# Kernel tuning notes

Measured on AMD Instinct MI355X. Metric: run time of the kernel, lower is better.

The kernel has to match this reference:

```python
import jax, jax.numpy as jnp
import numpy as np

DIM = 768
NUM_EXPERTS = 1536
EXPERT_DIM = 64
NOISE_SCALE = 0.1
B, H, W = 1, 64, 64
N = B * H * W


def setup_inputs() -> dict:
    key = jax.random.key(0)
    ks = jax.random.split(key, 6)
    scaled = lambda k, shape, fan_in: (jax.random.normal(k, shape, jnp.float32) / np.sqrt(fan_in)).astype(jnp.float32)
    return {
        "x": jax.random.normal(ks[0], (B, H, W, DIM), jnp.float32),
        "noise": jax.random.normal(ks[1], (N, NUM_EXPERTS), jnp.float32),
        "gate_w": scaled(ks[2], (NUM_EXPERTS, DIM), DIM),
        "gate_b": jnp.zeros((NUM_EXPERTS,), jnp.float32),
        "expert_w": scaled(ks[3], (NUM_EXPERTS, EXPERT_DIM, DIM), DIM),  # torch Linear weight layout (out, in)
        "expert_b": jnp.zeros((NUM_EXPERTS, EXPERT_DIM), jnp.float32),
        "proj_w": scaled(ks[4], (DIM, EXPERT_DIM), EXPERT_DIM),
        "proj_b": jnp.zeros((DIM,), jnp.float32),
    }


def reference(x, noise, gate_w, gate_b, expert_w, expert_b, proj_w, proj_b):
    orig_shape = x.shape
    xf = x.reshape(-1, orig_shape[-1])  # (N, DIM)
    # Noisy gating
    scores = xf @ gate_w.T + gate_b + noise * NOISE_SCALE  # (N, E)
    gate_weights = jax.nn.softmax(scores, axis=-1)
    top_w, top_i = jax.lax.top_k(gate_weights, 1)  # (N, 1), (N, 1)
    idx = top_i[:, 0]  # (N,)
    # Gather only the selected expert per token (same math as the redundant
    # dense all-expert compute followed by a gather in the original).
    w_sel = expert_w[idx]  # (N, EXPERT_DIM, DIM)
    b_sel = expert_b[idx]  # (N, EXPERT_DIM)
    y = jnp.einsum('nd,nod->no', xf, w_sel) + b_sel  # (N, EXPERT_DIM)
    out_flat = (y @ proj_w.T + proj_b) * top_w  # (N, DIM); top_w broadcasts (N,1)
    return out_flat.reshape(orig_shape)
```

## Files before the change

kernel.cpp:

```cpp
#include <hip/hip_runtime.h>
#include <hip/hip_bf16.h>

#define NT 4096
#define DIM 768
#define NE 1536
#define ED 64
#define GAP_THR 8e-3f

typedef __attribute__((ext_vector_type(8))) short short8v;
typedef __attribute__((ext_vector_type(4))) float f32x4;

__device__ __forceinline__ unsigned short f2bf(float f) {
  unsigned int u = __float_as_uint(f);
  unsigned int r = (u + 0x7fffu + ((u >> 16) & 1u)) >> 16;
  return (unsigned short)r;
}
__device__ __forceinline__ float bf2f(unsigned short h) {
  return __uint_as_float(((unsigned int)h) << 16);
}

__device__ __forceinline__ void gload16(const void* g, void* l) {
  __builtin_amdgcn_global_load_lds((const __attribute__((address_space(1))) void*)g,
                                   (__attribute__((address_space(3))) void*)l, 16, 0, 0);
}

__device__ __forceinline__ void top2_merge(float& m1, int& i1, float& m2, int& i2,
                                           float om1, int oi1, float om2, int oi2) {
  if (om1 > m1 || (om1 == m1 && oi1 < i1)) {
    if (m1 > om2 || (m1 == om2 && i1 < oi2)) { m2 = m1; i2 = i1; }
    else { m2 = om2; i2 = oi2; }
    m1 = om1; i1 = oi1;
  } else {
    if (om1 > m2 || (om1 == m2 && oi1 < i2)) { m2 = om1; i2 = oi1; }
  }
}

__global__ __launch_bounds__(256) void split_all(
    const float* __restrict__ x, const float* __restrict__ gw,
    unsigned short* __restrict__ xhi, unsigned short* __restrict__ xlo,
    unsigned short* __restrict__ ghi, unsigned short* __restrict__ glo,
    int* __restrict__ rc_cnt) {
  if (blockIdx.x == 0 && threadIdx.x == 0) *rc_cnt = 0;
  const int nx4 = NT * DIM / 4;
  const int ng4 = NE * DIM / 4;
  int i = blockIdx.x * 256 + threadIdx.x;
  const float* src; unsigned short* hi; unsigned short* lo; int j;
  if (i < nx4) { src = x; hi = xhi; lo = xlo; j = i; }
  else { j = i - nx4; if (j >= ng4) return; src = gw; hi = ghi; lo = glo; }
  float4 v = ((const float4*)src)[j];
  unsigned short h0 = f2bf(v.x), h1 = f2bf(v.y), h2 = f2bf(v.z), h3 = f2bf(v.w);
  ((ushort4*)hi)[j] = make_ushort4(h0, h1, h2, h3);
  ((ushort4*)lo)[j] = make_ushort4(f2bf(v.x - bf2f(h0)), f2bf(v.y - bf2f(h1)),
                                   f2bf(v.z - bf2f(h2)), f2bf(v.w - bf2f(h3)));
}

__global__ __launch_bounds__(256) void gate_mfma(
    const unsigned short* __restrict__ xhi, const unsigned short* __restrict__ xlo,
    const unsigned short* __restrict__ ghi, const unsigned short* __restrict__ glo,
    const float* __restrict__ gb, const float* __restrict__ noise,
    float4* __restrict__ part_a, int* __restrict__ part_i2) {
  __shared__ __align__(16) unsigned short sA[2 * 128 * 32];
  __shared__ __align__(16) unsigned short sB[2 * 128 * 32];
  const int tid = threadIdx.x;
  const int w = tid >> 6, lane = tid & 63;
  const int wr = w >> 1, wc = w & 1;
  const int bm = blockIdx.x, bn = blockIdx.y;
  const int fr = lane & 15;
  const int fg = lane >> 4;
  const int gsw = fg ^ ((fr >> 1) & 3);

  f32x4 acc[4][4];
#pragma unroll
  for (int i = 0; i < 4; i++)
#pragma unroll
    for (int j = 0; j < 4; j++) acc[i][j] = (f32x4){0.f, 0.f, 0.f, 0.f};

  const size_t arow = (size_t)bm * 128 * DIM;
  const size_t brow = (size_t)bn * 128 * DIM;
  const int sr_lo = tid >> 2;
  const int sg = (tid & 3) ^ ((tid >> 3) & 3);

  for (int kt = 0; kt < DIM; kt += 32) {
    __syncthreads();
#pragma unroll
    for (int h = 0; h < 2; h++) {
      const int r = h * 64 + sr_lo;
      const size_t asrc = arow + (size_t)r * DIM + kt + sg * 8;
      const size_t bsrc = brow + (size_t)r * DIM + kt + sg * 8;
      const int dofs = h * 2048 + w * 512;
      gload16(xhi + asrc, &sA[dofs]);
      gload16(xlo + asrc, &sA[4096 + dofs]);
      gload16(ghi + bsrc, &sB[dofs]);
      gload16(glo + bsrc, &sB[4096 + dofs]);
    }
    __syncthreads();

    short8v ah[4], al[4], bh[4], bl[4];
#pragma unroll
    for (int mf = 0; mf < 4; mf++) {
      int ro = (wr * 64 + mf * 16 + fr) * 32 + gsw * 8;
      ah[mf] = *(const short8v*)&sA[ro];
      al[mf] = *(const short8v*)&sA[4096 + ro];
    }
#pragma unroll
    for (int nf = 0; nf < 4; nf++) {
      int ro = (wc * 64 + nf * 16 + fr) * 32 + gsw * 8;
      bh[nf] = *(const short8v*)&sB[ro];
      bl[nf] = *(const short8v*)&sB[4096 + ro];
    }
#pragma unroll
    for (int mf = 0; mf < 4; mf++)
#pragma unroll
      for (int nf = 0; nf < 4; nf++) {
        f32x4 c = acc[mf][nf];
        c = __builtin_amdgcn_mfma_f32_16x16x32_bf16(ah[mf], bh[nf], c, 0, 0, 0);
        c = __builtin_amdgcn_mfma_f32_16x16x32_bf16(ah[mf], bl[nf], c, 0, 0, 0);
        c = __builtin_amdgcn_mfma_f32_16x16x32_bf16(al[mf], bh[nf], c, 0, 0, 0);
        acc[mf][nf] = c;
      }
  }

  const int gm0 = bm * 128 + wr * 64;
  const int gn0 = bn * 128 + wc * 64;
  const int chunk = bn * 2 + wc;
  int gcol[4]; float gbv[4];
#pragma unroll
  for (int nf = 0; nf < 4; nf++) { gcol[nf] = gn0 + nf * 16 + fr; gbv[nf] = gb[gcol[nf]]; }
#pragma unroll
  for (int mf = 0; mf < 4; mf++) {
    float sv[4][4];
#pragma unroll
    for (int nf = 0; nf < 4; nf++)
#pragma unroll
      for (int reg = 0; reg < 4; reg++) {
        int gm = gm0 + mf * 16 + fg * 4 + reg;
        sv[nf][reg] = acc[mf][nf][reg] + gbv[nf] + 0.1f * noise[(size_t)gm * NE + gcol[nf]];
      }
#pragma unroll
    for (int reg = 0; reg < 4; reg++) {
      float m1 = sv[0][reg]; int i1 = gcol[0];
      float m2 = -3e38f; int i2 = 0x7fffffff;
#pragma unroll
      for (int nf = 1; nf < 4; nf++) {
        float v = sv[nf][reg]; int ii = gcol[nf];
        if (v > m1 || (v == m1 && ii < i1)) { m2 = m1; i2 = i1; m1 = v; i1 = ii; }
        else if (v > m2 || (v == m2 && ii < i2)) { m2 = v; i2 = ii; }
      }
#pragma unroll
      for (int off = 1; off <= 8; off <<= 1) {
        float om1 = __shfl_xor(m1, off, 64); int oi1 = __shfl_xor(i1, off, 64);
        float om2 = __shfl_xor(m2, off, 64); int oi2 = __shfl_xor(i2, off, 64);
        top2_merge(m1, i1, m2, i2, om1, oi1, om2, oi2);
      }
      float ssum = 0.f;
#pragma unroll
      for (int nf = 0; nf < 4; nf++) ssum += __expf(sv[nf][reg] - m1);
#pragma unroll
      for (int off = 1; off <= 8; off <<= 1) ssum += __shfl_xor(ssum, off, 64);
      if (fr == 0) {
        int gm = gm0 + mf * 16 + fg * 4 + reg;
        part_a[(size_t)gm * 24 + chunk] = make_float4(m1, m2, ssum, __int_as_float(i1));
        part_i2[(size_t)gm * 24 + chunk] = i2;
      }
    }
  }
}

__global__ __launch_bounds__(256) void finalize(
    const float4* __restrict__ part_a, const int* __restrict__ part_i2,
    float* __restrict__ topw, int* __restrict__ idx,
    int* __restrict__ rc_count, int* __restrict__ rc_n, int* __restrict__ rc_i2) {
  const int wv = threadIdx.x >> 6, lane = threadIdx.x & 63;
  const int n = blockIdx.x * 4 + wv;
  float m1 = -3e38f, m2 = -3e38f, lm1 = -3e38f, lsum = 0.f;
  int i1 = 0x7fffffff, i2 = 0x7fffffff;
  if (lane < 24) {
    float4 pa = part_a[(size_t)n * 24 + lane];
    m1 = pa.x; m2 = pa.y; lsum = pa.z; i1 = __float_as_int(pa.w);
    i2 = part_i2[(size_t)n * 24 + lane];
    lm1 = pa.x;
  }
#pragma unroll
  for (int off = 1; off <= 32; off <<= 1) {
    float om1 = __shfl_xor(m1, off, 64); int oi1 = __shfl_xor(i1, off, 64);
    float om2 = __shfl_xor(m2, off, 64); int oi2 = __shfl_xor(i2, off, 64);
    top2_merge(m1, i1, m2, i2, om1, oi1, om2, oi2);
  }
  float contrib = (lane < 24) ? __expf(lm1 - m1) * lsum : 0.f;
#pragma unroll
  for (int off = 1; off <= 32; off <<= 1) contrib += __shfl_xor(contrib, off, 64);
  if (lane == 0) {
    topw[n] = 1.0f / contrib;
    idx[n] = i1;
    if (m1 - m2 < GAP_THR) {
      int p = atomicAdd(rc_count, 1);
      rc_n[p] = n; rc_i2[p] = i2;
    }
  }
}

__global__ __launch_bounds__(256) void recheck(
    const float* __restrict__ x, const float* __restrict__ gw,
    const float* __restrict__ gb, const float* __restrict__ noise,
    const int* __restrict__ rc_n, const int* __restrict__ rc_i2,
    const int* __restrict__ rc_count, int* __restrict__ idx) {
  __shared__ float r1[4], r2[4];
  const int cnt = *rc_count;
  const int tid = threadIdx.x;
  const int w = tid >> 6, lane = tid & 63;
  for (int t = blockIdx.x; t < cnt; t += gridDim.x) {
    const int n = rc_n[t];
    const int e1 = idx[n], e2 = rc_i2[t];
    const float* xr = x + (size_t)n * DIM;
    const float* w1 = gw + (size_t)e1 * DIM;
    const float* w2 = gw + (size_t)e2 * DIM;
    float p1 = 0.f, p2 = 0.f;
    for (int k = tid; k < DIM; k += 256) {
      float xv = xr[k];
      p1 += xv * w1[k];
      p2 += xv * w2[k];
    }
#pragma unroll
    for (int off = 32; off; off >>= 1) {
      p1 += __shfl_xor(p1, off, 64);
      p2 += __shfl_xor(p2, off, 64);
    }
    if (lane == 0) { r1[w] = p1; r2[w] = p2; }
    __syncthreads();
    if (tid == 0) {
      float s1 = r1[0] + r1[1] + r1[2] + r1[3] + gb[e1] + 0.1f * noise[(size_t)n * NE + e1];
      float s2 = r2[0] + r2[1] + r2[2] + r2[3] + gb[e2] + 0.1f * noise[(size_t)n * NE + e2];
      if (s2 > s1 || (s2 == s1 && e2 < e1)) idx[n] = e2;
    }
    __syncthreads();
  }
}

__global__ __launch_bounds__(256) void expert_y(
    const float* __restrict__ x, const float* __restrict__ ew,
    const float* __restrict__ eb, const int* __restrict__ idx,
    float* __restrict__ y) {
  const int e = blockIdx.x;
  __shared__ int toklist[128];
  __shared__ int ntok_s;
  const int tid = threadIdx.x;
  const int w = tid >> 6, lane = tid & 63;

  if (tid == 0) ntok_s = 0;
  __syncthreads();
  for (int q = tid; q < NT / 4; q += 256) {
    int4 v = ((const int4*)idx)[q];
    int n0 = q * 4;
    if (v.x == e) toklist[atomicAdd(&ntok_s, 1) & 127] = n0;
    if (v.y == e) toklist[atomicAdd(&ntok_s, 1) & 127] = n0 + 1;
    if (v.z == e) toklist[atomicAdd(&ntok_s, 1) & 127] = n0 + 2;
    if (v.w == e) toklist[atomicAdd(&ntok_s, 1) & 127] = n0 + 3;
  }
  __syncthreads();
  const int cnt = min(ntok_s, 128);
  if (cnt == 0) return;

  const float4* W4 = (const float4*)(ew + (size_t)e * ED * DIM);
  const float4* X4 = (const float4*)x;
  const float4* Wc = W4 + w * 16 * 192;

  for (int c0 = 0; c0 < cnt; c0 += 4) {
    const int cc = min(4, cnt - c0);
    const int tk0 = toklist[c0];
    const int tk1 = toklist[c0 + (1 < cc ? 1 : 0)];
    const int tk2 = toklist[c0 + (2 < cc ? 2 : 0)];
    const int tk3 = toklist[c0 + (3 < cc ? 3 : 0)];

    f32x4 x00 = *(const f32x4*)&X4[(size_t)tk0 * 192 + lane];
    f32x4 x01 = *(const f32x4*)&X4[(size_t)tk0 * 192 + 64 + lane];
    f32x4 x02 = *(const f32x4*)&X4[(size_t)tk0 * 192 + 128 + lane];
    f32x4 x10 = *(const f32x4*)&X4[(size_t)tk1 * 192 + lane];
    f32x4 x11 = *(const f32x4*)&X4[(size_t)tk1 * 192 + 64 + lane];
    f32x4 x12 = *(const f32x4*)&X4[(size_t)tk1 * 192 + 128 + lane];
    f32x4 x20 = *(const f32x4*)&X4[(size_t)tk2 * 192 + lane];
    f32x4 x21 = *(const f32x4*)&X4[(size_t)tk2 * 192 + 64 + lane];
    f32x4 x22 = *(const f32x4*)&X4[(size_t)tk2 * 192 + 128 + lane];
    f32x4 x30 = *(const f32x4*)&X4[(size_t)tk3 * 192 + lane];
    f32x4 x31 = *(const f32x4*)&X4[(size_t)tk3 * 192 + 64 + lane];
    f32x4 x32 = *(const f32x4*)&X4[(size_t)tk3 * 192 + 128 + lane];

    f32x4 wa0 = *(const f32x4*)&Wc[lane];
    f32x4 wa1 = *(const f32x4*)&Wc[64 + lane];
    f32x4 wa2 = *(const f32x4*)&Wc[128 + lane];
#pragma unroll
    for (int a = 0; a < 16; a++) {
      f32x4 wb0, wb1, wb2;
      if (a < 15) {
        wb0 = *(const f32x4*)&Wc[(a + 1) * 192 + lane];
        wb1 = *(const f32x4*)&Wc[(a + 1) * 192 + 64 + lane];
        wb2 = *(const f32x4*)&Wc[(a + 1) * 192 + 128 + lane];
      }
      float p0 = wa0.x * x00.x + wa0.y * x00.y + wa0.z * x00.z + wa0.w * x00.w
               + wa1.x * x01.x + wa1.y * x01.y + wa1.z * x01.z + wa1.w * x01.w
               + wa2.x * x02.x + wa2.y * x02.y + wa2.z * x02.z + wa2.w * x02.w;
      float p1 = wa0.x * x10.x + wa0.y * x10.y + wa0.z * x10.z + wa0.w * x10.w
               + wa1.x * x11.x + wa1.y * x11.y + wa1.z * x11.z + wa1.w * x11.w
               + wa2.x * x12.x + wa2.y * x12.y + wa2.z * x12.z + wa2.w * x12.w;
      float p2 = wa0.x * x20.x + wa0.y * x20.y + wa0.z * x20.z + wa0.w * x20.w
               + wa1.x * x21.x + wa1.y * x21.y + wa1.z * x21.z + wa1.w * x21.w
               + wa2.x * x22.x + wa2.y * x22.y + wa2.z * x22.z + wa2.w * x22.w;
      float p3 = wa0.x * x30.x + wa0.y * x30.y + wa0.z * x30.z + wa0.w * x30.w
               + wa1.x * x31.x + wa1.y * x31.y + wa1.z * x31.z + wa1.w * x31.w
               + wa2.x * x32.x + wa2.y * x32.y + wa2.z * x32.z + wa2.w * x32.w;

      const bool b0 = (lane & 1) != 0;
      float q0 = (b0 ? p1 : p0) + __shfl_xor(b0 ? p0 : p1, 1, 64);
      float q1 = (b0 ? p3 : p2) + __shfl_xor(b0 ? p2 : p3, 1, 64);
      const bool b1 = (lane & 2) != 0;
      float r = (b1 ? q1 : q0) + __shfl_xor(b1 ? q0 : q1, 2, 64);
      r += __shfl_xor(r, 4, 64);
      r += __shfl_xor(r, 8, 64);
      r += __shfl_xor(r, 16, 64);
      r += __shfl_xor(r, 32, 64);

      const int o = w * 16 + a;
      if (lane < cc) {
        y[(size_t)toklist[c0 + lane] * ED + o] = r + eb[e * ED + o];
      }
      wa0 = wb0; wa1 = wb1; wa2 = wb2;
    }
  }
}

__global__ __launch_bounds__(256) void proj_kernel(
    const float* __restrict__ y, const float* __restrict__ pw,
    const float* __restrict__ pb, const float* __restrict__ topw,
    float* __restrict__ out) {
  const int b = blockIdx.x;
  const int tid = threadIdx.x;
  __shared__ float4 ys4[8 * 16];
  __shared__ float tw[8];
  if (tid < 128) {
    int t = tid >> 4, q = tid & 15;
    ys4[tid] = ((const float4*)y)[((size_t)b * 8 + t) * 16 + q];
  }
  if (tid < 8) tw[tid] = topw[b * 8 + tid];
  __syncthreads();
  const float4* pw4 = (const float4*)pw;
#pragma unroll
  for (int c = 0; c < 3; c++) {
    int d = c * 256 + tid;
    float4 pwv[16];
#pragma unroll
    for (int q = 0; q < 16; q++) pwv[q] = pw4[(size_t)d * 16 + q];
    float pbv = pb[d];
    for (int t = 0; t < 8; t++) {
      const float4* yv4 = &ys4[t * 16];
      float s = 0.f;
#pragma unroll
      for (int q = 0; q < 16; q++) {
        float4 yv = yv4[q];
        s += pwv[q].x * yv.x + pwv[q].y * yv.y + pwv[q].z * yv.z + pwv[q].w * yv.w;
      }
      out[((size_t)b * 8 + t) * DIM + d] = (s + pbv) * tw[t];
    }
  }
}

extern "C" void kernel_launch(void* const* d_in, const int* in_sizes, int n_in,
                              void* d_out, int out_size, void* d_ws, size_t ws_size,
                              hipStream_t stream) {
  const float* x      = (const float*)d_in[0];
  const float* noise  = (const float*)d_in[1];
  const float* gate_w = (const float*)d_in[2];
  const float* gate_b = (const float*)d_in[3];
  const float* ew     = (const float*)d_in[4];
  const float* eb     = (const float*)d_in[5];
  const float* pw     = (const float*)d_in[6];
  const float* pb     = (const float*)d_in[7];
  float* out = (float*)d_out;

  char* ws = (char*)d_ws;
  unsigned short* xhi    = (unsigned short*)(ws);
  unsigned short* xlo    = (unsigned short*)(ws + 6291456);
  unsigned short* ghi    = (unsigned short*)(ws + 12582912);
  unsigned short* glo    = (unsigned short*)(ws + 14942208);
  float4*         part_a = (float4*)(ws + 17301504);
  int*            part_i2= (int*)  (ws + 18874368);
  float*          y      = (float*)(ws + 19267584);
  float*          topw   = (float*)(ws + 20316160);
  int*            idx    = (int*)  (ws + 20332544);
  int*            rc_cnt = (int*)  (ws + 20348928);
  int*            rc_n   = (int*)  (ws + 20349184);
  int*            rc_i2  = (int*)  (ws + 20365568);

  split_all<<<(NT * DIM / 4 + NE * DIM / 4 + 255) / 256, 256, 0, stream>>>(
      x, gate_w, xhi, xlo, ghi, glo, rc_cnt);
  gate_mfma<<<dim3(NT / 128, NE / 128), 256, 0, stream>>>(
      xhi, xlo, ghi, glo, gate_b, noise, part_a, part_i2);
  finalize<<<NT / 4, 256, 0, stream>>>(part_a, part_i2, topw, idx,
                                       rc_cnt, rc_n, rc_i2);
  recheck<<<64, 256, 0, stream>>>(x, gate_w, gate_b, noise, rc_n, rc_i2, rc_cnt, idx);
  expert_y<<<NE, 256, 0, stream>>>(x, ew, eb, idx, y);
  proj_kernel<<<NT / 8, 256, 0, stream>>>(y, pw, pb, topw, out);
}
```

Measured before the change: 246.5 us.

## Sort tokens by expert into 4-token groups and shrink gate GEMM tile

```diff
diff --git a/kernel.cpp b/kernel.cpp
--- a/kernel.cpp
+++ b/kernel.cpp
@@ -6,6 +6,7 @@
 #define NE 1536
 #define ED 64
 #define GAP_THR 8e-3f
+#define MAXG 2304
 
 typedef __attribute__((ext_vector_type(8))) short short8v;
 typedef __attribute__((ext_vector_type(4))) float f32x4;
@@ -39,8 +40,11 @@
     const float* __restrict__ x, const float* __restrict__ gw,
     unsigned short* __restrict__ xhi, unsigned short* __restrict__ xlo,
     unsigned short* __restrict__ ghi, unsigned short* __restrict__ glo,
-    int* __restrict__ rc_cnt) {
-  if (blockIdx.x == 0 && threadIdx.x == 0) *rc_cnt = 0;
+    int* __restrict__ rc_cnt, int* __restrict__ counts) {
+  if (blockIdx.x == 0) {
+    for (int j = threadIdx.x; j < NE; j += 256) counts[j] = 0;
+    if (threadIdx.x == 0) *rc_cnt = 0;
+  }
   const int nx4 = NT * DIM / 4;
   const int ng4 = NE * DIM / 4;
   int i = blockIdx.x * 256 + threadIdx.x;
@@ -59,59 +63,60 @@
     const unsigned short* __restrict__ ghi, const unsigned short* __restrict__ glo,
     const float* __restrict__ gb, const float* __restrict__ noise,
     float4* __restrict__ part_a, int* __restrict__ part_i2) {
-  __shared__ __align__(16) unsigned short sA[2 * 128 * 32];
+  __shared__ __align__(16) unsigned short sA[2 * 64 * 32];
   __shared__ __align__(16) unsigned short sB[2 * 128 * 32];
   const int tid = threadIdx.x;
   const int w = tid >> 6, lane = tid & 63;
-  const int wr = w >> 1, wc = w & 1;
   const int bm = blockIdx.x, bn = blockIdx.y;
   const int fr = lane & 15;
   const int fg = lane >> 4;
   const int gsw = fg ^ ((fr >> 1) & 3);
 
-  f32x4 acc[4][4];
+  f32x4 acc[4][2];
 #pragma unroll
   for (int i = 0; i < 4; i++)
 #pragma unroll
-    for (int j = 0; j < 4; j++) acc[i][j] = (f32x4){0.f, 0.f, 0.f, 0.f};
-
-  const size_t arow = (size_t)bm * 128 * DIM;
+    for (int j = 0; j < 2; j++) acc[i][j] = (f32x4){0.f, 0.f, 0.f, 0.f};
+
+  const size_t arow = (size_t)bm * 64 * DIM;
   const size_t brow = (size_t)bn * 128 * DIM;
-  const int sr_lo = tid >> 2;
-  const int sg = (tid & 3) ^ ((tid >> 3) & 3);
+  const int rA = tid >> 2;
+  const int sgA = (tid & 3) ^ ((rA >> 1) & 3);
+  const int sgB = (tid & 3) ^ ((tid >> 3) & 3);
 
   for (int kt = 0; kt < DIM; kt += 32) {
     __syncthreads();
-#pragma unroll
-    for (int h = 0; h < 2; h++) {
-      const int r = h * 64 + sr_lo;
-      const size_t asrc = arow + (size_t)r * DIM + kt + sg * 8;
-      const size_t bsrc = brow + (size_t)r * DIM + kt + sg * 8;
-      const int dofs = h * 2048 + w * 512;
-      gload16(xhi + asrc, &sA[dofs]);
-      gload16(xlo + asrc, &sA[4096 + dofs]);
-      gload16(ghi + bsrc, &sB[dofs]);
-      gload16(glo + bsrc, &sB[4096 + dofs]);
-    }
-    __syncthreads();
-
-    short8v ah[4], al[4], bh[4], bl[4];
+    {
+      const size_t asrc = arow + (size_t)rA * DIM + kt + sgA * 8;
+      gload16(xhi + asrc, &sA[w * 512]);
+      gload16(xlo + asrc, &sA[2048 + w * 512]);
+#pragma unroll
+      for (int h = 0; h < 2; h++) {
+        const int r = h * 64 + (tid >> 2);
+        const size_t bsrc = brow + (size_t)r * DIM + kt + sgB * 8;
+        gload16(ghi + bsrc, &sB[h * 2048 + w * 512]);
+        gload16(glo + bsrc, &sB[4096 + h * 2048 + w * 512]);
+      }
+    }
+    __syncthreads();
+
+    short8v ah[4], al[4], bh[2], bl[2];
 #pragma unroll
     for (int mf = 0; mf < 4; mf++) {
-      int ro = (wr * 64 + mf * 16 + fr) * 32 + gsw * 8;
+      int ro = (mf * 16 + fr) * 32 + gsw * 8;
       ah[mf] = *(const short8v*)&sA[ro];
-      al[mf] = *(const short8v*)&sA[4096 + ro];
-    }
-#pragma unroll
-    for (int nf = 0; nf < 4; nf++) {
-      int ro = (wc * 64 + nf * 16 + fr) * 32 + gsw * 8;
+      al[mf] = *(const short8v*)&sA[2048 + ro];
+    }
+#pragma unroll
+    for (int nf = 0; nf < 2; nf++) {
+      int ro = (w * 32 + nf * 16 + fr) * 32 + gsw * 8;
       bh[nf] = *(const short8v*)&sB[ro];
       bl[nf] = *(const short8v*)&sB[4096 + ro];
     }
 #pragma unroll
     for (int mf = 0; mf < 4; mf++)
 #pragma unroll
-      for (int nf = 0; nf < 4; nf++) {
+      for (int nf = 0; nf < 2; nf++) {
         f32x4 c = acc[mf][nf];
         c = __builtin_amdgcn_mfma_f32_16x16x32_bf16(ah[mf], bh[nf], c, 0, 0, 0);
         c = __builtin_amdgcn_mfma_f32_16x16x32_bf16(ah[mf], bl[nf], c, 0, 0, 0);
@@ -120,17 +125,17 @@
       }
   }
 
-  const int gm0 = bm * 128 + wr * 64;
-  const int gn0 = bn * 128 + wc * 64;
-  const int chunk = bn * 2 + wc;
-  int gcol[4]; float gbv[4];
-#pragma unroll
-  for (int nf = 0; nf < 4; nf++) { gcol[nf] = gn0 + nf * 16 + fr; gbv[nf] = gb[gcol[nf]]; }
+  const int gm0 = bm * 64;
+  const int gn0 = bn * 128 + w * 32;
+  const int chunk = bn * 4 + w;
+  int gcol[2]; float gbv[2];
+#pragma unroll
+  for (int nf = 0; nf < 2; nf++) { gcol[nf] = gn0 + nf * 16 + fr; gbv[nf] = gb[gcol[nf]]; }
 #pragma unroll
   for (int mf = 0; mf < 4; mf++) {
-    float sv[4][4];
-#pragma unroll
-    for (int nf = 0; nf < 4; nf++)
+    float sv[2][4];
+#pragma unroll
+    for (int nf = 0; nf < 2; nf++)
 #pragma unroll
       for (int reg = 0; reg < 4; reg++) {
         int gm = gm0 + mf * 16 + fg * 4 + reg;
@@ -140,11 +145,10 @@
     for (int reg = 0; reg < 4; reg++) {
       float m1 = sv[0][reg]; int i1 = gcol[0];
       float m2 = -3e38f; int i2 = 0x7fffffff;
-#pragma unroll
-      for (int nf = 1; nf < 4; nf++) {
-        float v = sv[nf][reg]; int ii = gcol[nf];
+      {
+        float v = sv[1][reg]; int ii = gcol[1];
         if (v > m1 || (v == m1 && ii < i1)) { m2 = m1; i2 = i1; m1 = v; i1 = ii; }
-        else if (v > m2 || (v == m2 && ii < i2)) { m2 = v; i2 = ii; }
+        else { m2 = v; i2 = ii; }
       }
 #pragma unroll
       for (int off = 1; off <= 8; off <<= 1) {
@@ -152,15 +156,13 @@
         float om2 = __shfl_xor(m2, off, 64); int oi2 = __shfl_xor(i2, off, 64);
         top2_merge(m1, i1, m2, i2, om1, oi1, om2, oi2);
       }
-      float ssum = 0.f;
-#pragma unroll
-      for (int nf = 0; nf < 4; nf++) ssum += __expf(sv[nf][reg] - m1);
+      float ssum = __expf(sv[0][reg] - m1) + __expf(sv[1][reg] - m1);
 #pragma unroll
       for (int off = 1; off <= 8; off <<= 1) ssum += __shfl_xor(ssum, off, 64);
       if (fr == 0) {
         int gm = gm0 + mf * 16 + fg * 4 + reg;
-        part_a[(size_t)gm * 24 + chunk] = make_float4(m1, m2, ssum, __int_as_float(i1));
-        part_i2[(size_t)gm * 24 + chunk] = i2;
+        part_a[(size_t)gm * 48 + chunk] = make_float4(m1, m2, ssum, __int_as_float(i1));
+        part_i2[(size_t)gm * 48 + chunk] = i2;
       }
     }
   }
@@ -168,16 +170,16 @@
 
 __global__ __launch_bounds__(256) void finalize(
     const float4* __restrict__ part_a, const int* __restrict__ part_i2,
-    float* __restrict__ topw, int* __restrict__ idx,
+    float* __restrict__ topw, int* __restrict__ idx, int* __restrict__ counts,
     int* __restrict__ rc_count, int* __restrict__ rc_n, int* __restrict__ rc_i2) {
   const int wv = threadIdx.x >> 6, lane = threadIdx.x & 63;
   const int n = blockIdx.x * 4 + wv;
   float m1 = -3e38f, m2 = -3e38f, lm1 = -3e38f, lsum = 0.f;
   int i1 = 0x7fffffff, i2 = 0x7fffffff;
-  if (lane < 24) {
-    float4 pa = part_a[(size_t)n * 24 + lane];
+  if (lane < 48) {
+    float4 pa = part_a[(size_t)n * 48 + lane];
     m1 = pa.x; m2 = pa.y; lsum = pa.z; i1 = __float_as_int(pa.w);
-    i2 = part_i2[(size_t)n * 24 + lane];
+    i2 = part_i2[(size_t)n * 48 + lane];
     lm1 = pa.x;
   }
 #pragma unroll
@@ -186,12 +188,13 @@
     float om2 = __shfl_xor(m2, off, 64); int oi2 = __shfl_xor(i2, off, 64);
     top2_merge(m1, i1, m2, i2, om1, oi1, om2, oi2);
   }
-  float contrib = (lane < 24) ? __expf(lm1 - m1) * lsum : 0.f;
+  float contrib = (lane < 48) ? __expf(lm1 - m1) * lsum : 0.f;
 #pragma unroll
   for (int off = 1; off <= 32; off <<= 1) contrib += __shfl_xor(contrib, off, 64);
   if (lane == 0) {
     topw[n] = 1.0f / contrib;
     idx[n] = i1;
+    atomicAdd(counts + i1, 1);
     if (m1 - m2 < GAP_THR) {
       int p = atomicAdd(rc_count, 1);
       rc_n[p] = n; rc_i2[p] = i2;
@@ -203,7 +206,7 @@
     const float* __restrict__ x, const float* __restrict__ gw,
     const float* __restrict__ gb, const float* __restrict__ noise,
     const int* __restrict__ rc_n, const int* __restrict__ rc_i2,
-    const int* __restrict__ rc_count, int* __restrict__ idx) {
+    const int* __restrict__ rc_count, int* __restrict__ idx, int* __restrict__ counts) {
   __shared__ float r1[4], r2[4];
   const int cnt = *rc_count;
   const int tid = threadIdx.x;
@@ -230,99 +233,142 @@
     if (tid == 0) {
       float s1 = r1[0] + r1[1] + r1[2] + r1[3] + gb[e1] + 0.1f * noise[(size_t)n * NE + e1];
       float s2 = r2[0] + r2[1] + r2[2] + r2[3] + gb[e2] + 0.1f * noise[(size_t)n * NE + e2];
-      if (s2 > s1 || (s2 == s1 && e2 < e1)) idx[n] = e2;
-    }
-    __syncthreads();
-  }
+      if (s2 > s1 || (s2 == s1 && e2 < e1)) {
+        idx[n] = e2;
+        atomicSub(counts + e1, 1);
+        atomicAdd(counts + e2, 1);
+      }
+    }
+    __syncthreads();
+  }
+}
+
+__global__ __launch_bounds__(256) void scan_offsets(
+    const int* __restrict__ counts, int* __restrict__ offs, int* __restrict__ cursor,
+    int* __restrict__ gdesc, int* __restrict__ ngroups) {
+  __shared__ int part[256];
+  __shared__ int part2[256];
+  const int t = threadIdx.x;
+  int loc[6];
+  int s = 0, s2 = 0;
+#pragma unroll
+  for (int j = 0; j < 6; j++) {
+    loc[j] = counts[t * 6 + j];
+    s += loc[j];
+    s2 += (loc[j] + 3) >> 2;
+  }
+  part[t] = s; part2[t] = s2;
+  __syncthreads();
+  for (int d = 1; d < 256; d <<= 1) {
+    int v1 = (t >= d) ? part[t - d] : 0;
+    int v2 = (t >= d) ? part2[t - d] : 0;
+    __syncthreads();
+    part[t] += v1; part2[t] += v2;
+    __syncthreads();
+  }
+  int excl = part[t] - s;
+  int excl2 = part2[t] - s2;
+#pragma unroll
+  for (int j = 0; j < 6; j++) {
+    const int e = t * 6 + j, c = loc[j];
+    offs[e] = excl;
+    cursor[e] = excl;
+    const int ng = (c + 3) >> 2;
+    for (int k = 0; k < ng; k++) {
+      gdesc[3 * (excl2 + k)]     = e;
+      gdesc[3 * (excl2 + k) + 1] = excl + 4 * k;
+      gdesc[3 * (excl2 + k) + 2] = min(4, c - 4 * k);
+    }
+    excl += c; excl2 += ng;
+  }
+  if (t == 255) *ngroups = part2[255];
+}
+
+__global__ __launch_bounds__(256) void scatter_tokens(
+    const int* __restrict__ idx, int* __restrict__ cursor, int* __restrict__ sorted) {
+  const int n = blockIdx.x * 256 + threadIdx.x;
+  int e = idx[n];
+  int pos = atomicAdd(cursor + e, 1);
+  sorted[pos] = n;
 }
 
 __global__ __launch_bounds__(256) void expert_y(
     const float* __restrict__ x, const float* __restrict__ ew,
-    const float* __restrict__ eb, const int* __restrict__ idx,
+    const float* __restrict__ eb, const int* __restrict__ sorted,
+    const int* __restrict__ gdesc, const int* __restrict__ ngroups,
     float* __restrict__ y) {
-  const int e = blockIdx.x;
-  __shared__ int toklist[128];
-  __shared__ int ntok_s;
+  const int g = blockIdx.x;
+  if (g >= *ngroups) return;
+  const int e    = gdesc[3 * g];
+  const int base = gdesc[3 * g + 1];
+  const int cc   = gdesc[3 * g + 2];
   const int tid = threadIdx.x;
   const int w = tid >> 6, lane = tid & 63;
 
-  if (tid == 0) ntok_s = 0;
-  __syncthreads();
-  for (int q = tid; q < NT / 4; q += 256) {
-    int4 v = ((const int4*)idx)[q];
-    int n0 = q * 4;
-    if (v.x == e) toklist[atomicAdd(&ntok_s, 1) & 127] = n0;
-    if (v.y == e) toklist[atomicAdd(&ntok_s, 1) & 127] = n0 + 1;
-    if (v.z == e) toklist[atomicAdd(&ntok_s, 1) & 127] = n0 + 2;
-    if (v.w == e) toklist[atomicAdd(&ntok_s, 1) & 127] = n0 + 3;
-  }
-  __syncthreads();
-  const int cnt = min(ntok_s, 128);
-  if (cnt == 0) return;
+  const int tk0 = sorted[base];
+  const int tk1 = sorted[base + (1 < cc ? 1 : 0)];
+  const int tk2 = sorted[base + (2 < cc ? 2 : 0)];
+  const int tk3 = sorted[base + (3 < cc ? 3 : 0)];
+  const int mytk = (lane == 0) ? tk0 : (lane == 1) ? tk1 : (lane == 2) ? tk2 : tk3;
 
   const float4* W4 = (const float4*)(ew + (size_t)e * ED * DIM);
   const float4* X4 = (const float4*)x;
   const float4* Wc = W4 + w * 16 * 192;
 
-  for (int c0 = 0; c0 < cnt; c0 += 4) {
-    const int cc = min(4, cnt - c0);
-    const int tk0 = toklist[c0];
-    const int tk1 = toklist[c0 + (1 < cc ? 1 : 0)];
-    const int tk2 = toklist[c0 + (2 < cc ? 2 : 0)];
-    const int tk3 = toklist[c0 + (3 < cc ? 3 : 0)];
-
-    f32x4 x00 = *(const f32x4*)&X4[(size_t)tk0 * 192 + lane];
-    f32x4 x01 = *(const f32x4*)&X4[(size_t)tk0 * 192 + 64 + lane];
-    f32x4 x02 = *(const f32x4*)&X4[(size_t)tk0 * 192 + 128 + lane];
-    f32x4 x10 = *(const f32x4*)&X4[(size_t)tk1 * 192 + lane];
-    f32x4 x11 = *(const f32x4*)&X4[(size_t)tk1 * 192 + 64 + lane];
-    f32x4 x12 = *(const f32x4*)&X4[(size_t)tk1 * 192 + 128 + lane];
-    f32x4 x20 = *(const f32x4*)&X4[(size_t)tk2 * 192 + lane];
-    f32x4 x21 = *(const f32x4*)&X4[(size_t)tk2 * 192 + 64 + lane];
-    f32x4 x22 = *(const f32x4*)&X4[(size_t)tk2 * 192 + 128 + lane];
-    f32x4 x30 = *(const f32x4*)&X4[(size_t)tk3 * 192 + lane];
-    f32x4 x31 = *(const f32x4*)&X4[(size_t)tk3 * 192 + 64 + lane];
-    f32x4 x32 = *(const f32x4*)&X4[(size_t)tk3 * 192 + 128 + lane];
-
-    f32x4 wa0 = *(const f32x4*)&Wc[lane];
-    f32x4 wa1 = *(const f32x4*)&Wc[64 + lane];
-    f32x4 wa2 = *(const f32x4*)&Wc[128 + lane];
-#pragma unroll
-    for (int a = 0; a < 16; a++) {
-      f32x4 wb0, wb1, wb2;
-      if (a < 15) {
-        wb0 = *(const f32x4*)&Wc[(a + 1) * 192 + lane];
-        wb1 = *(const f32x4*)&Wc[(a + 1) * 192 + 64 + lane];
-        wb2 = *(const f32x4*)&Wc[(a + 1) * 192 + 128 + lane];
-      }
-      float p0 = wa0.x * x00.x + wa0.y * x00.y + wa0.z * x00.z + wa0.w * x00.w
-               + wa1.x * x01.x + wa1.y * x01.y + wa1.z * x01.z + wa1.w * x01.w
-               + wa2.x * x02.x + wa2.y * x02.y + wa2.z * x02.z + wa2.w * x02.w;
-      float p1 = wa0.x * x10.x + wa0.y * x10.y + wa0.z * x10.z + wa0.w * x10.w
-               + wa1.x * x11.x + wa1.y * x11.y + wa1.z * x11.z + wa1.w * x11.w
-               + wa2.x * x12.x + wa2.y * x12.y + wa2.z * x12.z + wa2.w * x12.w;
-      float p2 = wa0.x * x20.x + wa0.y * x20.y + wa0.z * x20.z + wa0.w * x20.w
-               + wa1.x * x21.x + wa1.y * x21.y + wa1.z * x21.z + wa1.w * x21.w
-               + wa2.x * x22.x + wa2.y * x22.y + wa2.z * x22.z + wa2.w * x22.w;
-      float p3 = wa0.x * x30.x + wa0.y * x30.y + wa0.z * x30.z + wa0.w * x30.w
-               + wa1.x * x31.x + wa1.y * x31.y + wa1.z * x31.z + wa1.w * x31.w
-               + wa2.x * x32.x + wa2.y * x32.y + wa2.z * x32.z + wa2.w * x32.w;
-
-      const bool b0 = (lane & 1) != 0;
-      float q0 = (b0 ? p1 : p0) + __shfl_xor(b0 ? p0 : p1, 1, 64);
-      float q1 = (b0 ? p3 : p2) + __shfl_xor(b0 ? p2 : p3, 1, 64);
-      const bool b1 = (lane & 2) != 0;
-      float r = (b1 ? q1 : q0) + __shfl_xor(b1 ? q0 : q1, 2, 64);
-      r += __shfl_xor(r, 4, 64);
-      r += __shfl_xor(r, 8, 64);
-      r += __shfl_xor(r, 16, 64);
-      r += __shfl_xor(r, 32, 64);
-
-      const int o = w * 16 + a;
-      if (lane < cc) {
-        y[(size_t)toklist[c0 + lane] * ED + o] = r + eb[e * ED + o];
-      }
-      wa0 = wb0; wa1 = wb1; wa2 = wb2;
+  f32x4 x00 = *(const f32x4*)&X4[(size_t)tk0 * 192 + lane];
+  f32x4 x01 = *(const f32x4*)&X4[(size_t)tk0 * 192 + 64 + lane];
+  f32x4 x02 = *(const f32x4*)&X4[(size_t)tk0 * 192 + 128 + lane];
+  f32x4 x10 = *(const f32x4*)&X4[(size_t)tk1 * 192 + lane];
+  f32x4 x11 = *(const f32x4*)&X4[(size_t)tk1 * 192 + 64 + lane];
+  f32x4 x12 = *(const f32x4*)&X4[(size_t)tk1 * 192 + 128 + lane];
+  f32x4 x20 = *(const f32x4*)&X4[(size_t)tk2 * 192 + lane];
+  f32x4 x21 = *(const f32x4*)&X4[(size_t)tk2 * 192 + 64 + lane];
+  f32x4 x22 = *(const f32x4*)&X4[(size_t)tk2 * 192 + 128 + lane];
+  f32x4 x30 = *(const f32x4*)&X4[(size_t)tk3 * 192 + lane];
+  f32x4 x31 = *(const f32x4*)&X4[(size_t)tk3 * 192 + 64 + lane];
+  f32x4 x32 = *(const f32x4*)&X4[(size_t)tk3 * 192 + 128 + lane];
+
+  f32x4 wbuf[2][3];
+#pragma unroll
+  for (int j = 0; j < 3; j++) wbuf[0][j] = *(const f32x4*)&Wc[j * 64 + lane];
+#pragma unroll
+  for (int j = 0; j < 3; j++) wbuf[1][j] = *(const f32x4*)&Wc[192 + j * 64 + lane];
+
+#pragma unroll
+  for (int a = 0; a < 16; a++) {
+    const int cur = a & 1;
+    f32x4 wa0 = wbuf[cur][0], wa1 = wbuf[cur][1], wa2 = wbuf[cur][2];
+    if (a < 14) {
+      wbuf[cur][0] = *(const f32x4*)&Wc[(a + 2) * 192 + lane];
+      wbuf[cur][1] = *(const f32x4*)&Wc[(a + 2) * 192 + 64 + lane];
+      wbuf[cur][2] = *(const f32x4*)&Wc[(a + 2) * 192 + 128 + lane];
+    }
+    float p0 = wa0.x * x00.x + wa0.y * x00.y + wa0.z * x00.z + wa0.w * x00.w
+             + wa1.x * x01.x + wa1.y * x01.y + wa1.z * x01.z + wa1.w * x01.w
+             + wa2.x * x02.x + wa2.y * x02.y + wa2.z * x02.z + wa2.w * x02.w;
+    float p1 = wa0.x * x10.x + wa0.y * x10.y + wa0.z * x10.z + wa0.w * x10.w
+             + wa1.x * x11.x + wa1.y * x11.y + wa1.z * x11.z + wa1.w * x11.w
+             + wa2.x * x12.x + wa2.y * x12.y + wa2.z * x12.z + wa2.w * x12.w;
+    float p2 = wa0.x * x20.x + wa0.y * x20.y + wa0.z * x20.z + wa0.w * x20.w
+             + wa1.x * x21.x + wa1.y * x21.y + wa1.z * x21.z + wa1.w * x21.w
+             + wa2.x * x22.x + wa2.y * x22.y + wa2.z * x22.z + wa2.w * x22.w;
+    float p3 = wa0.x * x30.x + wa0.y * x30.y + wa0.z * x30.z + wa0.w * x30.w
+             + wa1.x * x31.x + wa1.y * x31.y + wa1.z * x31.z + wa1.w * x31.w
+             + wa2.x * x32.x + wa2.y * x32.y + wa2.z * x32.z + wa2.w * x32.w;
+
+    const bool b0 = (lane & 1) != 0;
+    float q0 = (b0 ? p1 : p0) + __shfl_xor(b0 ? p0 : p1, 1, 64);
+    float q1 = (b0 ? p3 : p2) + __shfl_xor(b0 ? p2 : p3, 1, 64);
+    const bool b1 = (lane & 2) != 0;
+    float r = (b1 ? q1 : q0) + __shfl_xor(b1 ? q0 : q1, 2, 64);
+    r += __shfl_xor(r, 4, 64);
+    r += __shfl_xor(r, 8, 64);
+    r += __shfl_xor(r, 16, 64);
+    r += __shfl_xor(r, 32, 64);
+
+    const int o = w * 16 + a;
+    if (lane < cc) {
+      y[(size_t)mytk * ED + o] = r + eb[e * ED + o];
     }
   }
 }
@@ -381,21 +427,30 @@
   unsigned short* ghi    = (unsigned short*)(ws + 12582912);
   unsigned short* glo    = (unsigned short*)(ws + 14942208);
   float4*         part_a = (float4*)(ws + 17301504);
-  int*            part_i2= (int*)  (ws + 18874368);
-  float*          y      = (float*)(ws + 19267584);
-  float*          topw   = (float*)(ws + 20316160);
-  int*            idx    = (int*)  (ws + 20332544);
-  int*            rc_cnt = (int*)  (ws + 20348928);
-  int*            rc_n   = (int*)  (ws + 20349184);
-  int*            rc_i2  = (int*)  (ws + 20365568);
+  int*            part_i2= (int*)  (ws + 20447232);
+  float*          y      = (float*)(ws + 21233664);
+  float*          topw   = (float*)(ws + 22282240);
+  int*            idx    = (int*)  (ws + 22298624);
+  int*            counts = (int*)  (ws + 22315008);
+  int*            rc_cnt = (int*)  (ws + 22321152);
+  int*            offs   = (int*)  (ws + 22321408);
+  int*            cursor = (int*)  (ws + 22327552);
+  int*            sorted = (int*)  (ws + 22333696);
+  int*            rc_n   = (int*)  (ws + 22350080);
+  int*            rc_i2  = (int*)  (ws + 22366464);
+  int*            ngroups= (int*)  (ws + 22382848);
+  int*            gdesc  = (int*)  (ws + 22383104);
 
   split_all<<<(NT * DIM / 4 + NE * DIM / 4 + 255) / 256, 256, 0, stream>>>(
-      x, gate_w, xhi, xlo, ghi, glo, rc_cnt);
-  gate_mfma<<<dim3(NT / 128, NE / 128), 256, 0, stream>>>(
+      x, gate_w, xhi, xlo, ghi, glo, rc_cnt, counts);
+  gate_mfma<<<dim3(NT / 64, NE / 128), 256, 0, stream>>>(
       xhi, xlo, ghi, glo, gate_b, noise, part_a, part_i2);
-  finalize<<<NT / 4, 256, 0, stream>>>(part_a, part_i2, topw, idx,
+  finalize<<<NT / 4, 256, 0, stream>>>(part_a, part_i2, topw, idx, counts,
                                        rc_cnt, rc_n, rc_i2);
-  recheck<<<64, 256, 0, stream>>>(x, gate_w, gate_b, noise, rc_n, rc_i2, rc_cnt, idx);
-  expert_y<<<NE, 256, 0, stream>>>(x, ew, eb, idx, y);
+  recheck<<<64, 256, 0, stream>>>(x, gate_w, gate_b, noise, rc_n, rc_i2, rc_cnt,
+                                  idx, counts);
+  scan_offsets<<<1, 256, 0, stream>>>(counts, offs, cursor, gdesc, ngroups);
+  scatter_tokens<<<NT / 256, 256, 0, stream>>>(idx, cursor, sorted);
+  expert_y<<<MAXG, 256, 0, stream>>>(x, ew, eb, sorted, gdesc, ngroups, y);
   proj_kernel<<<NT / 8, 256, 0, stream>>>(y, pw, pb, topw, out);
 }
```

After: 232.4 us. -5.7%, faster.
